# Optimization experiments

Measured on AMD Instinct MI355X. Metric: run time of the kernel, lower is better.

Reference implementation:

```python
import jax, jax.numpy as jnp
import numpy as np

B, L, H, TE = 256, 2048, 64, 64  # batch, seq len, hidden_size, num_time_enc_dims


def _lin_init(k, out_d, in_d):
    bound = 1.0 / np.sqrt(in_d)
    kw, kb = jax.random.split(k)
    w = jax.random.uniform(kw, (out_d, in_d), jnp.float32, -bound, bound)
    b = jax.random.uniform(kb, (out_d,), jnp.float32, -bound, bound)
    return w, b


def setup_inputs() -> dict:
    key = jax.random.key(0)
    ks = jax.random.split(key, 16)
    x_xy = jax.random.normal(ks[0], (B, L, 2), jnp.float32)
    mask = jax.random.bernoulli(ks[1], 0.8, (B, L, 1)).astype(jnp.float32)  # 0 => masked position
    x = jnp.concatenate([x_xy, mask], axis=-1)  # (B,L,3)
    t = jax.random.uniform(ks[2], (B, L, 1), jnp.float32)
    te_w1, te_b1 = _lin_init(ks[3], TE, 1)
    te_w2, te_b2 = _lin_init(ks[4], TE, TE)
    fproj_w, fproj_b = _lin_init(ks[5], H, 3 + TE)
    bproj_w, bproj_b = _lin_init(ks[6], H, 3 + TE)
    fwz, fbz = _lin_init(ks[7], H, H)
    fwh, fbh = _lin_init(ks[8], H, H)
    bwz, bbz = _lin_init(ks[9], H, H)
    bwh, bbh = _lin_init(ks[10], H, H)
    head_hidden = max((2 * H + TE) // 2, 128)  # = 128
    gh_w1, gh_b1 = _lin_init(ks[11], head_hidden, 2 * H + TE)
    gh_w2, gh_b2 = _lin_init(ks[12], 1, head_hidden)
    mask_token = jnp.array([0.0, 0.01], jnp.float32) + jnp.array([0.1, 0.001], jnp.float32) * jax.random.normal(ks[13], (2,), jnp.float32)
    return dict(x=x, t=t, mask_token=mask_token,
                te_w1=te_w1, te_b1=te_b1, te_w2=te_w2, te_b2=te_b2,
                fproj_w=fproj_w, fproj_b=fproj_b, bproj_w=bproj_w, bproj_b=bproj_b,
                fwz=fwz, fbz=fbz, fwh=fwh, fbh=fbh,
                bwz=bwz, bbz=bbz, bwh=bwh, bbh=bbh,
                gh_w1=gh_w1, gh_b1=gh_b1, gh_w2=gh_w2, gh_b2=gh_b2)


def _mingru_prestates(inp, wz, bz, wh, bh, reverse):
    # inp: (B,L,H). Returns the hidden state BEFORE each step's update, in
    # time order, matching the torch code which stores h_* before cell.step.
    z = jax.nn.sigmoid(jnp.einsum('blh,oh->blo', inp, wz) + bz)
    h_tilde = jnp.tanh(jnp.einsum('blh,oh->blo', inp, wh) + bh)

    def step(h, zh):
        z_t, ht_t = zh
        return (1.0 - z_t) * h + z_t * ht_t, h  # emit pre-update carry

    h0 = jnp.zeros((inp.shape[0], wz.shape[0]), inp.dtype)
    _, hs = jax.lax.scan(step, h0,
                         (jnp.swapaxes(z, 0, 1), jnp.swapaxes(h_tilde, 0, 1)),
                         reverse=reverse)
    return jnp.swapaxes(hs, 0, 1)  # (B,L,H)


def reference(x, t, mask_token,
              te_w1, te_b1, te_w2, te_b2,
              fproj_w, fproj_b, bproj_w, bproj_b,
              fwz, fbz, fwh, fbh,
              bwz, bbz, bwh, bbh,
              gh_w1, gh_b1, gh_w2, gh_b2):
    mask_chan = x[..., 2:3]                      # (B,L,1)
    masked_pos = mask_chan == 0
    x_first2 = jnp.where(masked_pos, mask_token.reshape(1, 1, 2), x[..., :2])
    x3 = jnp.concatenate([x_first2, mask_chan], axis=-1)  # (B,L,3)

    t_enc = jax.nn.relu(jnp.einsum('blk,ok->blo', t, te_w1) + te_b1)
    t_enc = jnp.einsum('blk,ok->blo', t_enc, te_w2) + te_b2  # (B,L,TE)

    x_cat = jnp.concatenate([x3, t_enc], axis=-1)  # (B,L,3+TE)

    inp_fwd = jnp.einsum('blk,ok->blo', x_cat, fproj_w) + fproj_b
    inp_bwd = jnp.einsum('blk,ok->blo', x_cat, bproj_w) + bproj_b

    h_fwd = _mingru_prestates(inp_fwd, fwz, fbz, fwh, fbh, reverse=False)  # state after steps 0..t-1
    h_bwd = _mingru_prestates(inp_bwd, bwz, bbz, bwh, bbh, reverse=True)   # state after steps L-1..t+1

    h_fwd_final = h_fwd[:, -1:, :]  # state after steps 0..L-2
    h_bwd_final = h_bwd[:, 0:1, :]  # state after steps L-1..1

    unmasked = mask_chan > 0
    h_fwd_apply = jnp.where(unmasked, h_fwd, h_fwd_final)
    h_bwd_apply = jnp.where(unmasked, h_bwd, h_bwd_final)

    h_bi = jnp.concatenate([h_fwd_apply, h_bwd_apply, t_enc], axis=-1)  # (B,L,2H+TE)
    hid = jax.nn.relu(jnp.einsum('blk,ok->blo', h_bi, gh_w1) + gh_b1)
    preds = jnp.einsum('blk,ok->blo', hid, gh_w2) + gh_b2  # (B,L,1)
    return preds
```

## Files before the change

kernel.cpp:

```cpp
#include <hip/hip_runtime.h>
#include <stdint.h>

#define NB 256
#define NL 2048

typedef __attribute__((ext_vector_type(8))) short short8;
typedef __attribute__((ext_vector_type(4))) float f32x4;
#define MFMA16(a,b,c) __builtin_amdgcn_mfma_f32_16x16x32_bf16(a,b,c,0,0,0)

static __device__ __forceinline__ unsigned short f2bf(float f) {
    union { float f; uint32_t u; } v; v.f = f;
    uint32_t u = v.u;
    uint32_t r = u + 0x7fffu + ((u >> 16) & 1u);
    return (unsigned short)(r >> 16);
}
static __device__ __forceinline__ float bflo(uint32_t u) {
    union { uint32_t u; float f; } v; v.u = u << 16; return v.f;
}
static __device__ __forceinline__ float bfhi(uint32_t u) {
    union { uint32_t u; float f; } v; v.u = u & 0xffff0000u; return v.f;
}
#if __has_builtin(__builtin_amdgcn_cvt_pk_bf16_f32)
typedef __attribute__((ext_vector_type(2))) __bf16 bf16x2_t;
static __device__ __forceinline__ uint32_t pk2(float lo, float hi) {
    union { bf16x2_t v; uint32_t u; } c;
    c.v = __builtin_amdgcn_cvt_pk_bf16_f32(lo, hi);
    return c.u;
}
static __device__ __forceinline__ unsigned short bf1(float v) {
    union { bf16x2_t v; uint32_t u; } c;
    c.v = __builtin_amdgcn_cvt_pk_bf16_f32(v, v);
    return (unsigned short)(c.u & 0xffffu);
}
#else
static __device__ __forceinline__ uint32_t pk2(float lo, float hi) {
    return ((uint32_t)f2bf(hi) << 16) | (uint32_t)f2bf(lo);
}
static __device__ __forceinline__ unsigned short bf1(float v) { return f2bf(v); }
#endif
static __device__ __forceinline__ short8 frag8(const float* p) {
    short8 r;
#pragma unroll
    for (int j = 0; j < 8; ++j) r[j] = (short)f2bf(p[j]);
    return r;
}

static __device__ __forceinline__ void barrier_lds() {
    asm volatile("s_waitcnt lgkmcnt(0)" ::: "memory");
    __builtin_amdgcn_s_barrier();
}

__global__ __launch_bounds__(256, 3) void prep_kernel(
    const float* __restrict__ x, const float* __restrict__ t,
    const float* __restrict__ mtok,
    const float* __restrict__ te_w1, const float* __restrict__ te_b1,
    const float* __restrict__ te_w2, const float* __restrict__ te_b2,
    const float* __restrict__ fpw, const float* __restrict__ fpb,
    const float* __restrict__ bpw, const float* __restrict__ bpb,
    const float* __restrict__ fwz, const float* __restrict__ fbz,
    const float* __restrict__ fwh, const float* __restrict__ fbh,
    const float* __restrict__ bwz, const float* __restrict__ bbz,
    const float* __restrict__ bwh, const float* __restrict__ bbh,
    int b0,
    uint32_t* __restrict__ abf,
    uint32_t* __restrict__ abb)
{
    __shared__ __align__(16) unsigned short s_te1[64*72];
    __shared__ __align__(16) unsigned short s_tenc[64*72];
    __shared__ __align__(16) unsigned short s_xa[64*40];
    __shared__ __align__(16) unsigned short s_inp[2][64*72];

    const int tid = threadIdx.x;
    const int w   = tid >> 6;
    const int l   = tid & 63;
    const int lq  = l >> 4;
    const int ln  = l & 15;

    short8 bte[2];
    {
        const float* row = te_w2 + (w*16 + ln)*64;
#pragma unroll
        for (int ks = 0; ks < 2; ++ks) bte[ks] = frag8(row + lq*8 + ks*32);
    }
    short8 bpj[2][3];
#pragma unroll
    for (int p = 0; p < 2; ++p) {
        const int g = 2*w + p;
        const float* PW = (g < 4) ? fpw : bpw;
        const float* row = PW + ((g & 3)*16 + ln)*67;
#pragma unroll
        for (int ks = 0; ks < 2; ++ks) {
            float tmp[8];
#pragma unroll
            for (int j = 0; j < 8; ++j) tmp[j] = row[3 + lq*8 + ks*32 + j];
            bpj[p][ks] = frag8(tmp);
        }
        {
            float tmp[8];
#pragma unroll
            for (int j = 0; j < 8; ++j) tmp[j] = (lq == 0 && j < 3) ? row[j] : 0.f;
            bpj[p][2] = frag8(tmp);
        }
    }
    const int wdir = w >> 1, wnp = w & 1;
    short8 bgz[2][2], bgh[2][2];
    float bias_gz[2], bias_gh[2];
    {
        const float* WZ = wdir ? bwz : fwz;
        const float* WH = wdir ? bwh : fwh;
        const float* BZ = wdir ? bbz : fbz;
        const float* BH = wdir ? bbh : fbh;
#pragma unroll
        for (int nt2 = 0; nt2 < 2; ++nt2) {
            const int nt = wnp*2 + nt2;
            const float* rz = WZ + (nt*16 + ln)*64;
            const float* rh = WH + (nt*16 + ln)*64;
#pragma unroll
            for (int ks = 0; ks < 2; ++ks) {
                bgz[nt2][ks] = frag8(rz + lq*8 + ks*32);
                bgh[nt2][ks] = frag8(rh + lq*8 + ks*32);
            }
            bias_gz[nt2] = BZ[nt*16 + ln];
            bias_gh[nt2] = BH[nt*16 + ln];
        }
    }
    const float bias_te = te_b2[w*16 + ln];
    float bias_pj[2];
#pragma unroll
    for (int p = 0; p < 2; ++p) {
        const int g = 2*w + p;
        bias_pj[p] = ((g < 4) ? fpb : bpb)[(g & 3)*16 + ln];
    }
    const float mt0 = mtok[0], mt1 = mtok[1];

    const int baseposl = blockIdx.x * 256;

    auto P0 = [&](int ch) {
        const int gbase = (b0 << 11) + baseposl + ch*64;
        const int pos = tid & 63;
        const float tv = t[gbase + pos];
        const int k0 = (tid >> 6) * 16;
        uint32_t* dst = (uint32_t*)(s_te1 + pos*72 + k0);
#pragma unroll
        for (int kk = 0; kk < 16; kk += 2) {
            float v0 = fmaxf(fmaf(tv, te_w1[k0+kk],   te_b1[k0+kk]),   0.f);
            float v1 = fmaxf(fmaf(tv, te_w1[k0+kk+1], te_b1[k0+kk+1]), 0.f);
            dst[kk >> 1] = pk2(v0, v1);
        }
        if (tid < 64) {
            const float* xp = x + (size_t)(gbase + tid)*3;
            const float mc = xp[2];
            const float x0 = (mc == 0.f) ? mt0 : xp[0];
            const float x1 = (mc == 0.f) ? mt1 : xp[1];
            uint32_t* xr = (uint32_t*)(s_xa + tid*40);
            xr[0] = pk2(x0, x1);
            xr[1] = pk2(mc, 0.f);
        }
    };
    auto G1 = [&]() {
        const int o = w*16 + ln;
#pragma unroll
        for (int mt = 0; mt < 4; ++mt) {
            f32x4 c = {0.f, 0.f, 0.f, 0.f};
#pragma unroll
            for (int ks = 0; ks < 2; ++ks) {
                const short8 a = *(const short8*)(s_te1 + (mt*16+ln)*72 + lq*8 + ks*32);
                c = MFMA16(a, bte[ks], c);
            }
#pragma unroll
            for (int r = 0; r < 4; ++r) {
                const int m = mt*16 + lq*4 + r;
                s_tenc[m*72 + o] = bf1(c[r] + bias_te);
            }
        }
    };
    auto G2 = [&]() {
#pragma unroll
        for (int mt = 0; mt < 4; ++mt) {
            short8 a0 = *(const short8*)(s_tenc + (mt*16+ln)*72 + lq*8);
            short8 a1 = *(const short8*)(s_tenc + (mt*16+ln)*72 + lq*8 + 32);
            short8 a2 = *(const short8*)(s_xa   + (mt*16+ln)*40 + lq*8);
#pragma unroll
            for (int p = 0; p < 2; ++p) {
                const int g = 2*w + p;
                const int dir = g >> 2;
                const int o = (g & 3)*16 + ln;
                f32x4 c = {0.f, 0.f, 0.f, 0.f};
                c = MFMA16(a0, bpj[p][0], c);
                c = MFMA16(a1, bpj[p][1], c);
                c = MFMA16(a2, bpj[p][2], c);
#pragma unroll
                for (int r = 0; r < 4; ++r) {
                    const int m = mt*16 + lq*4 + r;
                    s_inp[dir][m*72 + o] = bf1(c[r] + bias_pj[p]);
                }
            }
        }
    };
    auto G3 = [&](int ch) {
        const int chbase = baseposl + ch*64;
        const int ll0 = chbase & 2047;
        const int bl  = chbase >> 11;
        uint32_t* abD = (wdir ? abb : abf) + ((size_t)bl*NL + ll0)*64;
#pragma unroll
        for (int mt = 0; mt < 4; ++mt) {
            const short8 a0 = *(const short8*)(s_inp[wdir] + (mt*16+ln)*72 + lq*8);
            const short8 a1 = *(const short8*)(s_inp[wdir] + (mt*16+ln)*72 + lq*8 + 32);
#pragma unroll
            for (int nt2 = 0; nt2 < 2; ++nt2) {
                f32x4 cz = {0.f, 0.f, 0.f, 0.f};
                f32x4 ch2 = {0.f, 0.f, 0.f, 0.f};
                cz  = MFMA16(a0, bgz[nt2][0], cz);
                cz  = MFMA16(a1, bgz[nt2][1], cz);
                ch2 = MFMA16(a0, bgh[nt2][0], ch2);
                ch2 = MFMA16(a1, bgh[nt2][1], ch2);
                const int o = (wnp*2 + nt2)*16 + ln;
#pragma unroll
                for (int r = 0; r < 4; ++r) {
                    const float az = cz[r]  + bias_gz[nt2];
                    const float ah = ch2[r] + bias_gh[nt2];
                    const float z  = __builtin_amdgcn_rcpf(1.f + __expf(-az));
                    const float cc = fminf(fmaxf(ah, -15.f), 15.f);
                    const float e2 = __expf(2.f * cc);
                    const float th = 1.f - 2.f * __builtin_amdgcn_rcpf(e2 + 1.f);
                    abD[(size_t)(mt*16 + lq*4 + r)*64 + o] = pk2(1.f - z, z * th);
                }
            }
        }
    };

#pragma unroll
    for (int i = tid; i < 64*20; i += 256) {
        if ((i % 20) >= 2) ((uint32_t*)s_xa)[i] = 0;
    }
    P0(0);
    barrier_lds();
    G1();
    barrier_lds();
    G2();
    barrier_lds();
#pragma unroll 1
    for (int ch = 0; ch < 4; ++ch) {
        G3(ch);
        if (ch < 3) P0(ch + 1);
        barrier_lds();
        if (ch < 3) {
            G1();
            barrier_lds();
            G2();
            barrier_lds();
        }
    }
}

#define SSTR 129

__global__ __launch_bounds__(256) void scan3_kernel(
    const uint32_t* __restrict__ abf, const uint32_t* __restrict__ abb,
    unsigned short* __restrict__ hf, unsigned short* __restrict__ hb)
{
    __shared__ uint32_t s_seg[32*SSTR];
    __shared__ float s_A[8][33], s_B[8][33], s_Hin[8][33];
    __shared__ float s_H[32];

    const int rl  = blockIdx.x >> 2;
    const int dir = (blockIdx.x >> 1) & 1;
    const int h0  = (blockIdx.x & 1) * 32;
    const int tid = threadIdx.x;
    const int h   = tid & 31;
    const int q   = tid >> 5;

    const uint32_t* ab = (dir ? abb : abf) + (size_t)rl * NL * 64 + h0;
    unsigned short* out = (dir ? hb : hf) + (size_t)rl * NL * 64 + h0;

    if (tid < 32) s_H[tid] = 0.f;
    barrier_lds();

#pragma unroll 1
    for (int si = 0; si < 16; ++si) {
        const int s  = dir ? (15 - si) : si;
        const int l0 = s * 128;

#pragma unroll
        for (int rep = 0; rep < 16; ++rep) {
            const int idx = rep*256 + tid;
            const int hh = idx & 31;
            const int ll = idx >> 5;
            s_seg[hh*SSTR + ll] = ab[(size_t)(l0 + ll)*64 + hh];
        }
        barrier_lds();

        uint32_t regs[16];
        float A = 1.f, Bc = 0.f;
#pragma unroll
        for (int i = 0; i < 16; ++i) {
            const int g = q*16 + i;
            const int xx = dir ? (127 - g) : g;
            const uint32_t uab = s_seg[h*SSTR + xx];
            regs[i] = uab;
            Bc = fmaf(bflo(uab), Bc, bfhi(uab));
            A *= bflo(uab);
        }
        s_A[q][h] = A; s_B[q][h] = Bc;
        barrier_lds();

        if (tid < 32) {
            float H = s_H[tid];
#pragma unroll
            for (int qq = 0; qq < 8; ++qq) {
                s_Hin[qq][tid] = H;
                H = fmaf(s_A[qq][tid], H, s_B[qq][tid]);
            }
            s_H[tid] = H;
        }
        barrier_lds();

        float hv = s_Hin[q][h];
#pragma unroll
        for (int i = 0; i < 16; ++i) {
            const int g = q*16 + i;
            const int xx = dir ? (127 - g) : g;
            const uint32_t uab = regs[i];
            out[(size_t)(l0 + xx)*64 + h] = bf1(hv);
            hv = fmaf(bflo(uab), hv, bfhi(uab));
        }
        barrier_lds();
    }
}

__global__ __launch_bounds__(256, 3) void head_kernel(
    const float* __restrict__ x, const float* __restrict__ t,
    const float* __restrict__ te_w1, const float* __restrict__ te_b1,
    const float* __restrict__ te_w2, const float* __restrict__ te_b2,
    const unsigned short* __restrict__ hf, const unsigned short* __restrict__ hb,
    const float* __restrict__ w1, const float* __restrict__ b1,
    const float* __restrict__ w2, const float* __restrict__ b2,
    int b0,
    float* __restrict__ out)
{
    __shared__ __align__(16) unsigned short s_a[64*200];
    __shared__ __align__(16) unsigned short s_te1[64*72];
    __shared__ float s_part[4][64];
    __shared__ float s_mc[64];

    const int tid = threadIdx.x;
    const int w   = tid >> 6;
    const int l   = tid & 63;
    const int lq  = l >> 4;
    const int ln  = l & 15;

    short8 bw1[2][6];
    float b1v[2], w2v[2];
#pragma unroll
    for (int p = 0; p < 2; ++p) {
        const int o = (2*w + p)*16 + ln;
        const float* row = w1 + o*192;
#pragma unroll
        for (int ks = 0; ks < 6; ++ks) bw1[p][ks] = frag8(row + lq*8 + ks*32);
        b1v[p] = b1[o];
        w2v[p] = w2[o];
    }
    short8 bte[2];
    {
        const float* row = te_w2 + (w*16 + ln)*64;
#pragma unroll
        for (int ks = 0; ks < 2; ++ks) bte[ks] = frag8(row + lq*8 + ks*32);
    }
    const float bias_te = te_b2[w*16 + ln];
    const float bias2 = b2[0];

    const int baseposl = blockIdx.x * 256;

    auto A = [&](int ch) {
        const int gbase = (b0 << 11) + baseposl + ch*64;
        if (tid < 64) s_mc[tid] = x[(size_t)(gbase + tid)*3 + 2];
        const int pos = tid & 63;
        const float tv = t[gbase + pos];
        const int k0 = (tid >> 6) * 16;
        uint32_t* dst = (uint32_t*)(s_te1 + pos*72 + k0);
#pragma unroll
        for (int kk = 0; kk < 16; kk += 2) {
            float v0 = fmaxf(fmaf(tv, te_w1[k0+kk],   te_b1[k0+kk]),   0.f);
            float v1 = fmaxf(fmaf(tv, te_w1[k0+kk+1], te_b1[k0+kk+1]), 0.f);
            dst[kk >> 1] = pk2(v0, v1);
        }
    };
    auto Bp = [&](int ch) {
        const int chbase = baseposl + ch*64;
        const int ll0 = chbase & 2047;
        const int bl  = chbase >> 11;
        const size_t rowbase = (size_t)bl * NL * 64;
#pragma unroll
        for (int rep = 0; rep < 4; ++rep) {
            const int idx = rep*256 + tid;
            const int seg = idx >> 9;
            const int row = (idx >> 3) & 63;
            const int c   = idx & 7;
            const bool unm = s_mc[row] > 0.f;
            const uint4* src = (seg == 0)
                ? (const uint4*)(hf + rowbase + (size_t)(unm ? (ll0+row) : (NL-1))*64)
                : (const uint4*)(hb + rowbase + (size_t)(unm ? (ll0+row) : 0)*64);
            ((uint4*)s_a)[row*25 + seg*8 + c] = src[c];
        }
        const int o = w*16 + ln;
#pragma unroll
        for (int mt = 0; mt < 4; ++mt) {
            f32x4 c = {0.f, 0.f, 0.f, 0.f};
#pragma unroll
            for (int ks = 0; ks < 2; ++ks) {
                const short8 a = *(const short8*)(s_te1 + (mt*16+ln)*72 + lq*8 + ks*32);
                c = MFMA16(a, bte[ks], c);
            }
#pragma unroll
            for (int r = 0; r < 4; ++r) {
                const int m = mt*16 + lq*4 + r;
                s_a[m*200 + 128 + o] = bf1(c[r] + bias_te);
            }
        }
    };
    auto Cp = [&]() {
#pragma unroll
        for (int mt = 0; mt < 4; ++mt) {
            short8 af[6];
#pragma unroll
            for (int ks = 0; ks < 6; ++ks)
                af[ks] = *(const short8*)(s_a + (mt*16+ln)*200 + lq*8 + ks*32);
            float vs[4] = {0.f, 0.f, 0.f, 0.f};
#pragma unroll
            for (int p = 0; p < 2; ++p) {
                f32x4 c = {0.f, 0.f, 0.f, 0.f};
#pragma unroll
                for (int ks = 0; ks < 6; ++ks) c = MFMA16(af[ks], bw1[p][ks], c);
#pragma unroll
                for (int r = 0; r < 4; ++r)
                    vs[r] += fmaxf(c[r] + b1v[p], 0.f) * w2v[p];
            }
#pragma unroll
            for (int mask = 1; mask < 16; mask <<= 1) {
#pragma unroll
                for (int r = 0; r < 4; ++r)
                    vs[r] += __shfl_xor(vs[r], mask);
            }
            if (ln == 0) {
#pragma unroll
                for (int r = 0; r < 4; ++r)
                    s_part[w][mt*16 + lq*4 + r] = vs[r];
            }
        }
    };
    auto Dp = [&](int ch) {
        const int gbase = (b0 << 11) + baseposl + ch*64;
        if (tid < 64) {
            out[gbase + tid] = s_part[0][tid] + s_part[1][tid]
                             + s_part[2][tid] + s_part[3][tid] + bias2;
        }
    };

    A(0);
    barrier_lds();
#pragma unroll 1
    for (int ch = 0; ch < 4; ++ch) {
        Bp(ch);
        barrier_lds();
        Cp();
        barrier_lds();
        Dp(ch);
        if (ch < 3) A(ch + 1);
        barrier_lds();
    }
}

extern "C" void kernel_launch(void* const* d_in, const int* in_sizes, int n_in,
                              void* d_out, int out_size, void* d_ws, size_t ws_size,
                              hipStream_t stream)
{
    const float* x     = (const float*)d_in[0];
    const float* t     = (const float*)d_in[1];
    const float* mtok  = (const float*)d_in[2];
    const float* te_w1 = (const float*)d_in[3];
    const float* te_b1 = (const float*)d_in[4];
    const float* te_w2 = (const float*)d_in[5];
    const float* te_b2 = (const float*)d_in[6];
    const float* fpw   = (const float*)d_in[7];
    const float* fpb   = (const float*)d_in[8];
    const float* bpw   = (const float*)d_in[9];
    const float* bpb   = (const float*)d_in[10];
    const float* fwz   = (const float*)d_in[11];
    const float* fbz   = (const float*)d_in[12];
    const float* fwh   = (const float*)d_in[13];
    const float* fbh   = (const float*)d_in[14];
    const float* bwz   = (const float*)d_in[15];
    const float* bbz   = (const float*)d_in[16];
    const float* bwh   = (const float*)d_in[17];
    const float* bbh   = (const float*)d_in[18];
    const float* w1    = (const float*)d_in[19];
    const float* b1    = (const float*)d_in[20];
    const float* w2    = (const float*)d_in[21];
    const float* b2    = (const float*)d_in[22];

    const size_t per_b = 1572864ull;
    int Bg = NB;
    while ((size_t)Bg * per_b > ws_size && Bg > 1) Bg >>= 1;
    const int nG = NB / Bg;

    char* ws = (char*)d_ws;
    uint32_t*       abf  = (uint32_t*)(ws);
    uint32_t*       abb  = abf + (size_t)Bg * 64 * NL;
    unsigned short* hf   = (unsigned short*)(abb + (size_t)Bg * 64 * NL);
    unsigned short* hb   = hf + (size_t)Bg * NL * 64;

    for (int g = 0; g < nG; ++g) {
        const int b0 = g * Bg;

        prep_kernel<<<8 * Bg, 256, 0, stream>>>(
            x, t, mtok, te_w1, te_b1, te_w2, te_b2,
            fpw, fpb, bpw, bpb, fwz, fbz, fwh, fbh, bwz, bbz, bwh, bbh,
            b0, abf, abb);

        scan3_kernel<<<4 * Bg, 256, 0, stream>>>(abf, abb, hf, hb);

        head_kernel<<<8 * Bg, 256, 0, stream>>>(
            x, t, te_w1, te_b1, te_w2, te_b2,
            hf, hb, w1, b1, w2, b2, b0, (float*)d_out);
    }
}
```

Measured before the change: 370.9 us.

## Move gate GEMMs from prep into scan kernel, storing bf16 projections instead

```diff
diff --git a/kernel.cpp b/kernel.cpp
--- a/kernel.cpp
+++ b/kernel.cpp
@@ -57,13 +57,9 @@
     const float* __restrict__ te_w2, const float* __restrict__ te_b2,
     const float* __restrict__ fpw, const float* __restrict__ fpb,
     const float* __restrict__ bpw, const float* __restrict__ bpb,
-    const float* __restrict__ fwz, const float* __restrict__ fbz,
-    const float* __restrict__ fwh, const float* __restrict__ fbh,
-    const float* __restrict__ bwz, const float* __restrict__ bbz,
-    const float* __restrict__ bwh, const float* __restrict__ bbh,
     int b0,
-    uint32_t* __restrict__ abf,
-    uint32_t* __restrict__ abb)
+    unsigned short* __restrict__ inpF,
+    unsigned short* __restrict__ inpB)
 {
     __shared__ __align__(16) unsigned short s_te1[64*72];
     __shared__ __align__(16) unsigned short s_tenc[64*72];
@@ -100,28 +96,6 @@
 #pragma unroll
             for (int j = 0; j < 8; ++j) tmp[j] = (lq == 0 && j < 3) ? row[j] : 0.f;
             bpj[p][2] = frag8(tmp);
-        }
-    }
-    const int wdir = w >> 1, wnp = w & 1;
-    short8 bgz[2][2], bgh[2][2];
-    float bias_gz[2], bias_gh[2];
-    {
-        const float* WZ = wdir ? bwz : fwz;
-        const float* WH = wdir ? bwh : fwh;
-        const float* BZ = wdir ? bbz : fbz;
-        const float* BH = wdir ? bbh : fbh;
-#pragma unroll
-        for (int nt2 = 0; nt2 < 2; ++nt2) {
-            const int nt = wnp*2 + nt2;
-            const float* rz = WZ + (nt*16 + ln)*64;
-            const float* rh = WH + (nt*16 + ln)*64;
-#pragma unroll
-            for (int ks = 0; ks < 2; ++ks) {
-                bgz[nt2][ks] = frag8(rz + lq*8 + ks*32);
-                bgh[nt2][ks] = frag8(rh + lq*8 + ks*32);
-            }
-            bias_gz[nt2] = BZ[nt*16 + ln];
-            bias_gh[nt2] = BH[nt*16 + ln];
         }
     }
     const float bias_te = te_b2[w*16 + ln];
@@ -197,35 +171,22 @@
             }
         }
     };
-    auto G3 = [&](int ch) {
+    auto S = [&](int ch) {
         const int chbase = baseposl + ch*64;
         const int ll0 = chbase & 2047;
         const int bl  = chbase >> 11;
-        uint32_t* abD = (wdir ? abb : abf) + ((size_t)bl*NL + ll0)*64;
-#pragma unroll
-        for (int mt = 0; mt < 4; ++mt) {
-            const short8 a0 = *(const short8*)(s_inp[wdir] + (mt*16+ln)*72 + lq*8);
-            const short8 a1 = *(const short8*)(s_inp[wdir] + (mt*16+ln)*72 + lq*8 + 32);
-#pragma unroll
-            for (int nt2 = 0; nt2 < 2; ++nt2) {
-                f32x4 cz = {0.f, 0.f, 0.f, 0.f};
-                f32x4 ch2 = {0.f, 0.f, 0.f, 0.f};
-                cz  = MFMA16(a0, bgz[nt2][0], cz);
-                cz  = MFMA16(a1, bgz[nt2][1], cz);
-                ch2 = MFMA16(a0, bgh[nt2][0], ch2);
-                ch2 = MFMA16(a1, bgh[nt2][1], ch2);
-                const int o = (wnp*2 + nt2)*16 + ln;
-#pragma unroll
-                for (int r = 0; r < 4; ++r) {
-                    const float az = cz[r]  + bias_gz[nt2];
-                    const float ah = ch2[r] + bias_gh[nt2];
-                    const float z  = __builtin_amdgcn_rcpf(1.f + __expf(-az));
-                    const float cc = fminf(fmaxf(ah, -15.f), 15.f);
-                    const float e2 = __expf(2.f * cc);
-                    const float th = 1.f - 2.f * __builtin_amdgcn_rcpf(e2 + 1.f);
-                    abD[(size_t)(mt*16 + lq*4 + r)*64 + o] = pk2(1.f - z, z * th);
-                }
-            }
+        uint32_t* dstF = (uint32_t*)inpF + ((size_t)bl*NL + ll0)*32;
+        uint32_t* dstB = (uint32_t*)inpB + ((size_t)bl*NL + ll0)*32;
+        const uint32_t* srcW = (const uint32_t*)s_inp;
+#pragma unroll
+        for (int rep = 0; rep < 16; ++rep) {
+            const int idx = rep*256 + tid;
+            const int d   = idx >> 11;
+            const int rem = idx & 2047;
+            const int ll  = rem >> 5;
+            const int dw  = rem & 31;
+            const uint32_t v = srcW[d*2304 + ll*36 + dw];
+            (d ? dstB : dstF)[ll*32 + dw] = v;
         }
     };
 
@@ -241,7 +202,7 @@
     barrier_lds();
 #pragma unroll 1
     for (int ch = 0; ch < 4; ++ch) {
-        G3(ch);
+        S(ch);
         if (ch < 3) P0(ch + 1);
         barrier_lds();
         if (ch < 3) {
@@ -255,38 +216,88 @@
 
 #define SSTR 129
 
-__global__ __launch_bounds__(256) void scan3_kernel(
-    const uint32_t* __restrict__ abf, const uint32_t* __restrict__ abb,
+__global__ __launch_bounds__(512, 2) void scan3_kernel(
+    const unsigned short* __restrict__ inpf, const unsigned short* __restrict__ inpb,
+    const float* __restrict__ fwz, const float* __restrict__ fbz,
+    const float* __restrict__ fwh, const float* __restrict__ fbh,
+    const float* __restrict__ bwz, const float* __restrict__ bbz,
+    const float* __restrict__ bwh, const float* __restrict__ bbh,
     unsigned short* __restrict__ hf, unsigned short* __restrict__ hb)
 {
-    __shared__ uint32_t s_seg[32*SSTR];
-    __shared__ float s_A[8][33], s_B[8][33], s_Hin[8][33];
-    __shared__ float s_H[32];
-
-    const int rl  = blockIdx.x >> 2;
-    const int dir = (blockIdx.x >> 1) & 1;
-    const int h0  = (blockIdx.x & 1) * 32;
+    __shared__ uint32_t s_seg[64*SSTR];
+    __shared__ float s_A[8][65], s_B[8][65], s_Hin[8][65];
+    __shared__ float s_H[64];
+
+    const int rl  = blockIdx.x >> 1;
+    const int dir = blockIdx.x & 1;
     const int tid = threadIdx.x;
-    const int h   = tid & 31;
-    const int q   = tid >> 5;
-
-    const uint32_t* ab = (dir ? abb : abf) + (size_t)rl * NL * 64 + h0;
-    unsigned short* out = (dir ? hb : hf) + (size_t)rl * NL * 64 + h0;
-
-    if (tid < 32) s_H[tid] = 0.f;
+    const int h   = tid & 63;
+    const int q   = tid >> 6;
+    const int lq  = h >> 4;
+    const int ln  = h & 15;
+
+    const unsigned short* inp = (dir ? inpb : inpf) + (size_t)rl * NL * 64;
+    unsigned short* out = (dir ? hb : hf) + (size_t)rl * NL * 64;
+
+    const float* WZ = dir ? bwz : fwz;
+    const float* WH = dir ? bwh : fwh;
+    const float* BZ = dir ? bbz : fbz;
+    const float* BH = dir ? bbh : fbh;
+
+    short8 bz[4][2], bh[4][2];
+    float biz[4], bih[4];
+#pragma unroll
+    for (int nt = 0; nt < 4; ++nt) {
+        const float* rz = WZ + (nt*16 + ln)*64;
+        const float* rh = WH + (nt*16 + ln)*64;
+#pragma unroll
+        for (int ks = 0; ks < 2; ++ks) {
+            bz[nt][ks] = frag8(rz + lq*8 + ks*32);
+            bh[nt][ks] = frag8(rh + lq*8 + ks*32);
+        }
+        biz[nt] = BZ[nt*16 + ln];
+        bih[nt] = BH[nt*16 + ln];
+    }
+
+    if (tid < 64) s_H[tid] = 0.f;
+
+    short8 a0c, a1c;
+    {
+        const int s0 = dir ? 15 : 0;
+        const unsigned short* p = inp + (size_t)(s0*128 + q*16 + ln)*64 + lq*8;
+        a0c = *(const short8*)(p);
+        a1c = *(const short8*)(p + 32);
+    }
+    short8 a0n = a0c, a1n = a1c;
     barrier_lds();
 
 #pragma unroll 1
     for (int si = 0; si < 16; ++si) {
-        const int s  = dir ? (15 - si) : si;
-        const int l0 = s * 128;
-
-#pragma unroll
-        for (int rep = 0; rep < 16; ++rep) {
-            const int idx = rep*256 + tid;
-            const int hh = idx & 31;
-            const int ll = idx >> 5;
-            s_seg[hh*SSTR + ll] = ab[(size_t)(l0 + ll)*64 + hh];
+        const int s = dir ? (15 - si) : si;
+        if (si < 15) {
+            const int sn = dir ? (14 - si) : (si + 1);
+            const unsigned short* p = inp + (size_t)(sn*128 + q*16 + ln)*64 + lq*8;
+            a0n = *(const short8*)(p);
+            a1n = *(const short8*)(p + 32);
+        }
+#pragma unroll
+        for (int nt = 0; nt < 4; ++nt) {
+            f32x4 cz  = {0.f, 0.f, 0.f, 0.f};
+            f32x4 ch2 = {0.f, 0.f, 0.f, 0.f};
+            cz  = MFMA16(a0c, bz[nt][0], cz);
+            cz  = MFMA16(a1c, bz[nt][1], cz);
+            ch2 = MFMA16(a0c, bh[nt][0], ch2);
+            ch2 = MFMA16(a1c, bh[nt][1], ch2);
+#pragma unroll
+            for (int r = 0; r < 4; ++r) {
+                const float az = cz[r]  + biz[nt];
+                const float ah = ch2[r] + bih[nt];
+                const float z  = __builtin_amdgcn_rcpf(1.f + __expf(-az));
+                const float cc = fminf(fmaxf(ah, -15.f), 15.f);
+                const float e2 = __expf(2.f * cc);
+                const float th = 1.f - 2.f * __builtin_amdgcn_rcpf(e2 + 1.f);
+                s_seg[(nt*16 + ln)*SSTR + q*16 + lq*4 + r] = pk2(1.f - z, z * th);
+            }
         }
         barrier_lds();
 
@@ -304,7 +315,7 @@
         s_A[q][h] = A; s_B[q][h] = Bc;
         barrier_lds();
 
-        if (tid < 32) {
+        if (tid < 64) {
             float H = s_H[tid];
 #pragma unroll
             for (int qq = 0; qq < 8; ++qq) {
@@ -316,6 +327,7 @@
         barrier_lds();
 
         float hv = s_Hin[q][h];
+        const int l0 = s * 128;
 #pragma unroll
         for (int i = 0; i < 16; ++i) {
             const int g = q*16 + i;
@@ -325,6 +337,7 @@
             hv = fmaf(bflo(uab), hv, bfhi(uab));
         }
         barrier_lds();
+        a0c = a0n; a1c = a1n;
     }
 }
 
@@ -498,26 +511,26 @@
     const float* w2    = (const float*)d_in[21];
     const float* b2    = (const float*)d_in[22];
 
-    const size_t per_b = 1572864ull;
+    const size_t per_b = 1048576ull;
     int Bg = NB;
     while ((size_t)Bg * per_b > ws_size && Bg > 1) Bg >>= 1;
     const int nG = NB / Bg;
 
     char* ws = (char*)d_ws;
-    uint32_t*       abf  = (uint32_t*)(ws);
-    uint32_t*       abb  = abf + (size_t)Bg * 64 * NL;
-    unsigned short* hf   = (unsigned short*)(abb + (size_t)Bg * 64 * NL);
-    unsigned short* hb   = hf + (size_t)Bg * NL * 64;
+    unsigned short* inpf = (unsigned short*)ws;
+    unsigned short* inpb = inpf + (size_t)Bg * NL * 64;
+    unsigned short* hf   = inpb + (size_t)Bg * NL * 64;
+    unsigned short* hb   = hf   + (size_t)Bg * NL * 64;
 
     for (int g = 0; g < nG; ++g) {
         const int b0 = g * Bg;
 
         prep_kernel<<<8 * Bg, 256, 0, stream>>>(
             x, t, mtok, te_w1, te_b1, te_w2, te_b2,
-            fpw, fpb, bpw, bpb, fwz, fbz, fwh, fbh, bwz, bbz, bwh, bbh,
-            b0, abf, abb);
-
-        scan3_kernel<<<4 * Bg, 256, 0, stream>>>(abf, abb, hf, hb);
+            fpw, fpb, bpw, bpb, b0, inpf, inpb);
+
+        scan3_kernel<<<2 * Bg, 512, 0, stream>>>(
+            inpf, inpb, fwz, fbz, fwh, fbh, bwz, bbz, bwh, bbh, hf, hb);
 
         head_kernel<<<8 * Bg, 256, 0, stream>>>(
             x, t, te_w1, te_b1, te_w2, te_b2,
```

Result: faster. 334.4 us (-9.9%).
